# Performance work log

Measured on AMD Instinct MI355X. Metric: run time of the kernel, lower is better.

Reference implementation:

```python
import jax, jax.numpy as jnp
import numpy as np

N, E, T = 10000, 160000, 1600000
D, C, H = 256, 64, 1024  # d_model, d_message/channels, 4*d_model ffn hidden


def setup_inputs() -> dict:
    key = jax.random.key(0)
    ks = jax.random.split(key, 20)
    rn = lambda k, s, sc=1.0: jax.random.normal(k, s, dtype=jnp.float32) * sc
    return {
        "x": rn(ks[0], (N, D)),
        "y": rn(ks[1], (E, D)),
        "r": rn(ks[2], (E, 3)),
        "src": jax.random.randint(ks[3], (E,), 0, N),
        "dst": jax.random.randint(ks[4], (E,), 0, N),
        "tsrc": jax.random.randint(ks[5], (T,), 0, E),
        "tdst": jax.random.randint(ks[6], (T,), 0, E),
        "W_src": rn(ks[7], (D, C), 0.05), "b_src": rn(ks[8], (C,), 0.05),
        "W_dst": rn(ks[9], (D, C), 0.05), "b_dst": rn(ks[10], (C,), 0.05),
        "W_edge": rn(ks[11], (D, C), 0.05), "b_edge": rn(ks[12], (C,), 0.05),
        "attn": rn(ks[13], (C,), 0.05),
        "W1": rn(ks[14], (C, H), 0.05), "b1": rn(ks[15], (H,), 0.05),
        "W2": rn(ks[16], (H, D), 0.05), "b2": rn(ks[17], (D,), 0.05),
    }


def reference(x, y, r, src, dst, tsrc, tdst,
              W_src, b_src, W_dst, b_dst, W_edge, b_edge,
              attn, W1, b1, W2, b2):
    # per-bond message: xij = Lin_src(x)[src] + Lin_dst(x)[dst] + Lin_edge(y)  -> (E, C)
    xij = (x @ W_src + b_src)[src] + (x @ W_dst + b_dst)[dst] + (y @ W_edge + b_edge)

    # triplet angle cosine via normalized (negated) bond vectors  -> (T,)
    rnorm = -r / jnp.linalg.norm(r, axis=1, keepdims=True)
    cos_jik = jnp.clip(jnp.sum(rnorm[tsrc] * rnorm[tdst], axis=-1), -1.0 + 1e-6, 1.0 - 1e-6)

    # Chebyshev expansion: T_n(cos) = cos(n * arccos(cos))  -> (T, C)
    n = jnp.arange(C, dtype=jnp.float32)
    z_jik = jnp.cos(n[None, :] * jnp.arccos(cos_jik)[:, None])

    # triplet feature and attention logit
    e_jik = jax.nn.silu(z_jik + xij[tsrc] + xij[tdst])          # (T, C)
    logits = e_jik @ attn                                        # (T,)

    # segment softmax over triplets grouped by destination bond (edge_softmax)
    mx = jax.ops.segment_max(logits, tdst, num_segments=E)
    ex = jnp.exp(logits - mx[tdst])
    den = jax.ops.segment_sum(ex, tdst, num_segments=E)
    a = ex / den[tdst]                                           # (T,)

    # attention-weighted scatter-sum of neighbor bond features  -> (E, C)
    ft = jax.ops.segment_sum(xij[tsrc] * a[:, None], tdst, num_segments=E)

    # feedforward: Linear -> SiLU -> Linear  -> (E, D)
    return jax.nn.silu(ft @ W1 + b1) @ W2 + b2
```

## Files before the change

### kernel.cpp

```cpp
#include <hip/hip_runtime.h>

#define N_NODES 10000
#define N_EDGES 160000
#define N_TRI   1600000
#define DM      256
#define CH      64
#define HH      1024

typedef short bf16x8 __attribute__((ext_vector_type(8)));
typedef float f32x4  __attribute__((ext_vector_type(4)));

__device__ __forceinline__ unsigned short f2bf(float f) {
  unsigned int u = __float_as_uint(f);
  u += 0x7fff + ((u >> 16) & 1);
  return (unsigned short)(u >> 16);
}

__global__ __launch_bounds__(256) void k_node_proj(
    const float* __restrict__ x, const float* __restrict__ Ws, const float* __restrict__ bs,
    const float* __restrict__ Wd, const float* __restrict__ bd,
    float* __restrict__ xs, float* __restrict__ xd) {
  __shared__ float xl[4][DM];
  int tid = threadIdx.x;
  int n0 = blockIdx.x * 4;
  for (int i = tid; i < 4 * DM; i += 256) xl[i >> 8][i & 255] = x[n0 * DM + i];
  __syncthreads();
  int c = tid & 63, g = tid >> 6;
  float as = bs[c], ad = bd[c];
  for (int d = 0; d < DM; d++) {
    float xv = xl[g][d];
    as += xv * Ws[d * CH + c];
    ad += xv * Wd[d * CH + c];
  }
  int n = n0 + g;
  xs[n * CH + c] = as;
  xd[n * CH + c] = ad;
}

__global__ __launch_bounds__(256) void k_edge_proj(
    const float* __restrict__ y, const float* __restrict__ We, const float* __restrict__ be,
    const float* __restrict__ xs, const float* __restrict__ xd,
    const int* __restrict__ src, const int* __restrict__ dst,
    float* __restrict__ xij) {
  __shared__ float yl[16][DM];
  int tid = threadIdx.x;
  int e0 = blockIdx.x * 16;
  for (int i = tid; i < 16 * DM; i += 256) yl[i >> 8][i & 255] = y[e0 * DM + i];
  __syncthreads();
  int c = tid & 63, g = tid >> 6;
  float acc[4];
#pragma unroll
  for (int s = 0; s < 4; s++) acc[s] = be[c];
  for (int d = 0; d < DM; d += 4) {
    float w0 = We[(d + 0) * CH + c];
    float w1 = We[(d + 1) * CH + c];
    float w2 = We[(d + 2) * CH + c];
    float w3 = We[(d + 3) * CH + c];
#pragma unroll
    for (int s = 0; s < 4; s++) {
      const float4 yv = *(const float4*)&yl[g * 4 + s][d];
      acc[s] += yv.x * w0 + yv.y * w1 + yv.z * w2 + yv.w * w3;
    }
  }
#pragma unroll
  for (int s = 0; s < 4; s++) {
    int e = e0 + g * 4 + s;
    xij[e * CH + c] = acc[s] + xs[src[e] * CH + c] + xd[dst[e] * CH + c];
  }
}

__global__ void k_rnorm(const float* __restrict__ r, float4* __restrict__ rn4) {
  int e = blockIdx.x * 256 + threadIdx.x;
  if (e >= N_EDGES) return;
  float a = r[e * 3 + 0], b = r[e * 3 + 1], c = r[e * 3 + 2];
  float inv = rsqrtf(a * a + b * b + c * c);
  rn4[e] = (float4){-a * inv, -b * inv, -c * inv, 0.f};
}

__global__ __launch_bounds__(256) void k_theta(
    const float4* __restrict__ rn4, const int* __restrict__ tsrc, const int* __restrict__ tdst,
    float* __restrict__ theta) {
  int t = blockIdx.x * 256 + threadIdx.x;
  if (t >= N_TRI) return;
  float4 a = rn4[tsrc[t]];
  float4 b = rn4[tdst[t]];
  float c = a.x * b.x + a.y * b.y + a.z * b.z;
  c = fminf(fmaxf(c, -1.0f + 1e-6f), 1.0f - 1e-6f);
  theta[t] = acosf(c);
}

__global__ void k_hist(const int* __restrict__ tdst, int* __restrict__ cnt) {
  int t = blockIdx.x * 256 + threadIdx.x;
  if (t < N_TRI) atomicAdd(&cnt[tdst[t]], 1);
}

__global__ __launch_bounds__(256) void k_scan_sum(const int* __restrict__ cnt,
                                                  int* __restrict__ bsum, int n) {
  __shared__ int s[256];
  int b = blockIdx.x, tid = threadIdx.x;
  int tot = 0;
#pragma unroll
  for (int i = 0; i < 8; i++) {
    int idx = b * 2048 + i * 256 + tid;
    if (idx < n) tot += cnt[idx];
  }
  s[tid] = tot;
  __syncthreads();
  for (int off = 128; off > 0; off >>= 1) {
    if (tid < off) s[tid] += s[tid + off];
    __syncthreads();
  }
  if (tid == 0) bsum[b] = s[0];
}

__global__ void k_scan_top(int* __restrict__ bsum, int nb, int* __restrict__ start_last) {
  if (threadIdx.x == 0) {
    int run = 0;
    for (int i = 0; i < nb; i++) {
      int v = bsum[i];
      bsum[i] = run;
      run += v;
    }
    *start_last = run;
  }
}

__global__ __launch_bounds__(256) void k_scan_apply(const int* __restrict__ cnt,
                                                    const int* __restrict__ bsum,
                                                    int* __restrict__ start,
                                                    int* __restrict__ cur, int n) {
  __shared__ int s[256];
  int b = blockIdx.x, tid = threadIdx.x;
  int base = b * 2048 + tid * 8;
  int loc[8];
  int tot = 0;
#pragma unroll
  for (int i = 0; i < 8; i++) {
    int idx = base + i;
    int v = (idx < n) ? cnt[idx] : 0;
    loc[i] = tot;
    tot += v;
  }
  s[tid] = tot;
  __syncthreads();
  for (int off = 1; off < 256; off <<= 1) {
    int t2 = 0;
    if (tid >= off) t2 = s[tid - off];
    __syncthreads();
    if (tid >= off) s[tid] += t2;
    __syncthreads();
  }
  int excl = s[tid] - tot + bsum[b];
#pragma unroll
  for (int i = 0; i < 8; i++) {
    int idx = base + i;
    if (idx < n) {
      int v = excl + loc[i];
      start[idx] = v;
      cur[idx] = v;
    }
  }
}

__global__ void k_scatter(const int* __restrict__ tdst, int* __restrict__ cur,
                          int* __restrict__ sorted) {
  int t = blockIdx.x * 256 + threadIdx.x;
  if (t < N_TRI) {
    int p = atomicAdd(&cur[tdst[t]], 1);
    sorted[p] = t;
  }
}

__global__ __launch_bounds__(256) void k_attn_ft(
    const int* __restrict__ start, const int* __restrict__ sorted,
    const float* __restrict__ theta, const int* __restrict__ tsrc,
    const float* __restrict__ xij, const float* __restrict__ attn,
    unsigned short* __restrict__ ft) {
  int tid = threadIdx.x;
  int e = blockIdx.x * 4 + (tid >> 6);
  int lane = tid & 63;
  float lanef = (float)lane;
  int beg = start[e], end = start[e + 1];
  int deg = end - beg;
  float xd = xij[e * CH + lane];
  float av = attn[lane];
  float m = -1e30f, den = 0.f, acc = 0.f;
  if (deg > 0 && deg <= 64) {
    int ts_ = 0;
    float th_ = 0.f;
    if (lane < deg) {
      int t = sorted[beg + lane];
      ts_ = tsrc[t];
      th_ = theta[t];
    }
    int ts_cur = __shfl(ts_, 0);
    float th_cur = __shfl(th_, 0);
    float xs_cur = xij[ts_cur * CH + lane];
    for (int i = 0; i < deg; i++) {
      float th_nxt = 0.f, xs_nxt = 0.f;
      if (i + 1 < deg) {
        int ts_nxt = __shfl(ts_, i + 1);
        th_nxt = __shfl(th_, i + 1);
        xs_nxt = xij[ts_nxt * CH + lane];
      }
      float v = __cosf(th_cur * lanef) + xs_cur + xd;
      float sv = v / (1.0f + __expf(-v));
      float contrib = sv * av;
#pragma unroll
      for (int off = 32; off; off >>= 1) contrib += __shfl_xor(contrib, off);
      float mn = fmaxf(m, contrib);
      float scale = __expf(m - mn);
      float p = __expf(contrib - mn);
      den = den * scale + p;
      acc = acc * scale + p * xs_cur;
      m = mn;
      th_cur = th_nxt;
      xs_cur = xs_nxt;
    }
  } else if (deg > 64) {
    for (int i = 0; i < deg; i++) {
      int t = sorted[beg + i];
      int ts = tsrc[t];
      float th = theta[t];
      float xs = xij[ts * CH + lane];
      float v = __cosf(th * lanef) + xs + xd;
      float sv = v / (1.0f + __expf(-v));
      float contrib = sv * av;
#pragma unroll
      for (int off = 32; off; off >>= 1) contrib += __shfl_xor(contrib, off);
      float mn = fmaxf(m, contrib);
      float scale = __expf(m - mn);
      float p = __expf(contrib - mn);
      den = den * scale + p;
      acc = acc * scale + p * xs;
      m = mn;
    }
  }
  ft[e * CH + lane] = f2bf(deg > 0 ? acc / den : 0.f);
}

__global__ __launch_bounds__(256) void k_prep_w1p(const float* __restrict__ W1,
                                                  unsigned short* __restrict__ W1P) {
  int idx = blockIdx.x * 256 + threadIdx.x;
  int k = idx & 63, row = idx >> 6;
  int i = row & 15, t = (row >> 4) & 1, hb = row >> 5;
  int hidden = hb * 32 + ((i >> 2) << 3) + (t << 2) + (i & 3);
  W1P[idx] = f2bf(W1[k * HH + hidden]);
}

__global__ __launch_bounds__(256) void k_prep_w2t(const float* __restrict__ W2,
                                                  unsigned short* __restrict__ W2T) {
  int idx = blockIdx.x * 256 + threadIdx.x;
  int n = idx >> 10, k = idx & 1023;
  W2T[idx] = f2bf(W2[k * DM + n]);
}

__global__ __launch_bounds__(256, 3) void k_ffn_mfma5(
    const unsigned short* __restrict__ ft, const unsigned short* __restrict__ W1P,
    const float* __restrict__ b1, const unsigned short* __restrict__ W2T,
    const float* __restrict__ b2, float* __restrict__ out) {
  __shared__ __align__(16) unsigned short hbuf[2][4 * 64 * 8];
  int tid = threadIdx.x;
  int w = tid >> 6, lane = tid & 63;
  int l16 = lane & 15, q = lane >> 4;
  int e0 = blockIdx.x * 64;

  bf16x8 ftf[2];
#pragma unroll
  for (int s = 0; s < 2; s++)
    ftf[s] = *(const bf16x8*)&ft[(size_t)(e0 + w * 16 + l16) * CH + s * 32 + q * 8];

  f32x4 acc[4][4];
#pragma unroll
  for (int mt = 0; mt < 4; mt++)
#pragma unroll
    for (int nt = 0; nt < 4; nt++) acc[mt][nt] = (f32x4){0.f, 0.f, 0.f, 0.f};

  bf16x8 w1f[2][2];
#pragma unroll
  for (int t = 0; t < 2; t++)
#pragma unroll
    for (int s = 0; s < 2; s++)
      w1f[t][s] = *(const bf16x8*)&W1P[(size_t)(t * 16 + l16) * 64 + s * 32 + q * 8];

  bf16x8 bwc[4];
#pragma unroll
  for (int nt = 0; nt < 4; nt++)
    bwc[nt] = *(const bf16x8*)&W2T[(size_t)(w * 64 + nt * 16 + l16) * HH + q * 8];

  int p = 0;
  for (int hb = 0; hb < 32; hb++) {
    int hbn = (hb < 31) ? hb + 1 : 31;
    bf16x8 bwn[4];
#pragma unroll
    for (int nt = 0; nt < 4; nt++)
      bwn[nt] = *(const bf16x8*)&W2T[(size_t)(w * 64 + nt * 16 + l16) * HH + hbn * 32 + q * 8];
    bf16x8 w1n[2][2];
#pragma unroll
    for (int t = 0; t < 2; t++)
#pragma unroll
      for (int s = 0; s < 2; s++)
        w1n[t][s] = *(const bf16x8*)&W1P[(size_t)((hbn * 2 + t) * 16 + l16) * 64 + s * 32 + q * 8];

    f32x4 h0 = (f32x4){0.f, 0.f, 0.f, 0.f};
    f32x4 h1 = (f32x4){0.f, 0.f, 0.f, 0.f};
    h0 = __builtin_amdgcn_mfma_f32_16x16x32_bf16(w1f[0][0], ftf[0], h0, 0, 0, 0);
    h0 = __builtin_amdgcn_mfma_f32_16x16x32_bf16(w1f[0][1], ftf[1], h0, 0, 0, 0);
    h1 = __builtin_amdgcn_mfma_f32_16x16x32_bf16(w1f[1][0], ftf[0], h1, 0, 0, 0);
    h1 = __builtin_amdgcn_mfma_f32_16x16x32_bf16(w1f[1][1], ftf[1], h1, 0, 0, 0);

    const float4 bv0 = *(const float4*)&b1[hb * 32 + q * 8];
    const float4 bv1 = *(const float4*)&b1[hb * 32 + q * 8 + 4];
    float v0 = h0[0] + bv0.x, v1 = h0[1] + bv0.y, v2 = h0[2] + bv0.z, v3 = h0[3] + bv0.w;
    float u0 = h1[0] + bv1.x, u1 = h1[1] + bv1.y, u2 = h1[2] + bv1.z, u3 = h1[3] + bv1.w;
    float s0 = v0 / (1.f + __expf(-v0)), s1 = v1 / (1.f + __expf(-v1));
    float s2 = v2 / (1.f + __expf(-v2)), s3 = v3 / (1.f + __expf(-v3));
    float t0 = u0 / (1.f + __expf(-u0)), t1 = u1 / (1.f + __expf(-u1));
    float t2 = u2 / (1.f + __expf(-u2)), t3 = u3 / (1.f + __expf(-u3));
    union { bf16x8 v; unsigned int u[4]; } pa;
    pa.u[0] = ((unsigned int)f2bf(s1) << 16) | f2bf(s0);
    pa.u[1] = ((unsigned int)f2bf(s3) << 16) | f2bf(s2);
    pa.u[2] = ((unsigned int)f2bf(t1) << 16) | f2bf(t0);
    pa.u[3] = ((unsigned int)f2bf(t3) << 16) | f2bf(t2);
    *(bf16x8*)&hbuf[p][(w * 64 + lane) * 8] = pa.v;

    __syncthreads();

    bf16x8 pam[4];
#pragma unroll
    for (int mt = 0; mt < 4; mt++)
      pam[mt] = *(const bf16x8*)&hbuf[p][(mt * 64 + lane) * 8];
#pragma unroll
    for (int nt = 0; nt < 4; nt++)
#pragma unroll
      for (int mt = 0; mt < 4; mt++)
        acc[mt][nt] = __builtin_amdgcn_mfma_f32_16x16x32_bf16(pam[mt], bwc[nt], acc[mt][nt], 0, 0, 0);

#pragma unroll
    for (int nt = 0; nt < 4; nt++) bwc[nt] = bwn[nt];
#pragma unroll
    for (int t = 0; t < 2; t++)
#pragma unroll
      for (int s = 0; s < 2; s++) w1f[t][s] = w1n[t][s];
    p ^= 1;
  }

#pragma unroll
  for (int nt = 0; nt < 4; nt++) {
    int col = w * 64 + nt * 16 + l16;
    float b2v = b2[col];
#pragma unroll
    for (int mt = 0; mt < 4; mt++) {
      int erow = e0 + mt * 16 + q * 4;
#pragma unroll
      for (int r = 0; r < 4; r++)
        out[(size_t)(erow + r) * DM + col] = acc[mt][nt][r] + b2v;
    }
  }
}

extern "C" void kernel_launch(void* const* d_in, const int* in_sizes, int n_in,
                              void* d_out, int out_size, void* d_ws, size_t ws_size,
                              hipStream_t stream) {
  (void)in_sizes; (void)n_in; (void)out_size; (void)ws_size;
  const float* x      = (const float*)d_in[0];
  const float* y      = (const float*)d_in[1];
  const float* r      = (const float*)d_in[2];
  const int*   src    = (const int*)d_in[3];
  const int*   dst    = (const int*)d_in[4];
  const int*   tsrc   = (const int*)d_in[5];
  const int*   tdst   = (const int*)d_in[6];
  const float* W_src  = (const float*)d_in[7];
  const float* b_src  = (const float*)d_in[8];
  const float* W_dst  = (const float*)d_in[9];
  const float* b_dst  = (const float*)d_in[10];
  const float* W_edge = (const float*)d_in[11];
  const float* b_edge = (const float*)d_in[12];
  const float* attn   = (const float*)d_in[13];
  const float* W1     = (const float*)d_in[14];
  const float* b1     = (const float*)d_in[15];
  const float* W2     = (const float*)d_in[16];
  const float* b2     = (const float*)d_in[17];
  float* out = (float*)d_out;

  char* wsp = (char*)d_ws;
  auto alloc = [&](size_t bytes) -> char* {
    char* p = wsp;
    wsp += (bytes + 255) & ~(size_t)255;
    return p;
  };
  float* xs     = (float*)alloc((size_t)N_NODES * CH * 4);
  float* xd     = (float*)alloc((size_t)N_NODES * CH * 4);
  float* xij    = (float*)alloc((size_t)N_EDGES * CH * 4);
  float4* rn4   = (float4*)alloc((size_t)N_EDGES * 16);
  float* theta  = (float*)alloc((size_t)N_TRI * 4);
  int*   cnt    = (int*)alloc((size_t)N_EDGES * 4);
  int*   start  = (int*)alloc((size_t)(N_EDGES + 1) * 4);
  int*   cur    = (int*)alloc((size_t)N_EDGES * 4);
  int*   bsum   = (int*)alloc(1024 * 4);
  int*   sorted = (int*)alloc((size_t)N_TRI * 4);
  unsigned short* ftb = (unsigned short*)alloc((size_t)N_EDGES * CH * 2);
  unsigned short* W1P = (unsigned short*)alloc((size_t)CH * HH * 2);
  unsigned short* W2T = (unsigned short*)alloc((size_t)HH * DM * 2);

  const int NB = (N_EDGES + 2047) / 2048;

  k_prep_w1p<<<(CH * HH) / 256, 256, 0, stream>>>(W1, W1P);
  k_prep_w2t<<<(HH * DM) / 256, 256, 0, stream>>>(W2, W2T);

  k_node_proj<<<N_NODES / 4, 256, 0, stream>>>(x, W_src, b_src, W_dst, b_dst, xs, xd);
  k_rnorm<<<N_EDGES / 256, 256, 0, stream>>>(r, rn4);
  k_edge_proj<<<N_EDGES / 16, 256, 0, stream>>>(y, W_edge, b_edge, xs, xd, src, dst, xij);
  k_theta<<<N_TRI / 256, 256, 0, stream>>>(rn4, tsrc, tdst, theta);

  hipMemsetAsync(cnt, 0, (size_t)N_EDGES * 4, stream);
  k_hist<<<N_TRI / 256, 256, 0, stream>>>(tdst, cnt);
  k_scan_sum<<<NB, 256, 0, stream>>>(cnt, bsum, N_EDGES);
  k_scan_top<<<1, 64, 0, stream>>>(bsum, NB, &start[N_EDGES]);
  k_scan_apply<<<NB, 256, 0, stream>>>(cnt, bsum, start, cur, N_EDGES);
  k_scatter<<<N_TRI / 256, 256, 0, stream>>>(tdst, cur, sorted);

  k_attn_ft<<<N_EDGES / 4, 256, 0, stream>>>(start, sorted, theta, tsrc, xij, attn, ftb);
  k_ffn_mfma5<<<N_EDGES / 64, 256, 0, stream>>>(ftb, W1P, b1, W2T, b2, out);
}
```

Measured before the change: 1.244 ms.

## Split fused FFN into two GEMM kernels with chunked hidden buffer

The fused FFN kernel, which computed the hidden activation per 64-edge tile and immediately consumed it through shared memory with a barrier each step, is replaced by two kernels per 40000-edge chunk. The first writes the bf16 SiLU hidden activations to a global workspace in MFMA fragment layout. The second reads them back and does the W2 GEMM, with the output columns split across two blocks. This removes the per-step __syncthreads and exposes more parallelism, but adds a global round trip of the hidden tensor (about 80 MB per chunk) and extra kernel launches.

```diff
diff --git a/kernel.cpp b/kernel.cpp
--- a/kernel.cpp
+++ b/kernel.cpp
@@ -6,6 +6,7 @@
 #define DM      256
 #define CH      64
 #define HH      1024
+#define ECHUNK  40000
 
 typedef short bf16x8 __attribute__((ext_vector_type(8)));
 typedef float f32x4  __attribute__((ext_vector_type(4)));
@@ -255,99 +256,92 @@
   W2T[idx] = f2bf(W2[k * DM + n]);
 }
 
-__global__ __launch_bounds__(256, 3) void k_ffn_mfma5(
+__global__ __launch_bounds__(256) void k_ffn_g1(
     const unsigned short* __restrict__ ft, const unsigned short* __restrict__ W1P,
-    const float* __restrict__ b1, const unsigned short* __restrict__ W2T,
-    const float* __restrict__ b2, float* __restrict__ out) {
-  __shared__ __align__(16) unsigned short hbuf[2][4 * 64 * 8];
+    const float* __restrict__ b1, unsigned short* __restrict__ hpk) {
   int tid = threadIdx.x;
   int w = tid >> 6, lane = tid & 63;
   int l16 = lane & 15, q = lane >> 4;
-  int e0 = blockIdx.x * 64;
-
-  bf16x8 ftf[2];
-#pragma unroll
-  for (int s = 0; s < 2; s++)
-    ftf[s] = *(const bf16x8*)&ft[(size_t)(e0 + w * 16 + l16) * CH + s * 32 + q * 8];
-
-  f32x4 acc[4][4];
+  int tile = blockIdx.x;
+  int e0 = tile * 64;
+
+  bf16x8 ftf[4][2];
 #pragma unroll
   for (int mt = 0; mt < 4; mt++)
 #pragma unroll
-    for (int nt = 0; nt < 4; nt++) acc[mt][nt] = (f32x4){0.f, 0.f, 0.f, 0.f};
-
-  bf16x8 w1f[2][2];
-#pragma unroll
-  for (int t = 0; t < 2; t++)
-#pragma unroll
     for (int s = 0; s < 2; s++)
-      w1f[t][s] = *(const bf16x8*)&W1P[(size_t)(t * 16 + l16) * 64 + s * 32 + q * 8];
-
-  bf16x8 bwc[4];
-#pragma unroll
-  for (int nt = 0; nt < 4; nt++)
-    bwc[nt] = *(const bf16x8*)&W2T[(size_t)(w * 64 + nt * 16 + l16) * HH + q * 8];
-
-  int p = 0;
-  for (int hb = 0; hb < 32; hb++) {
-    int hbn = (hb < 31) ? hb + 1 : 31;
-    bf16x8 bwn[4];
-#pragma unroll
-    for (int nt = 0; nt < 4; nt++)
-      bwn[nt] = *(const bf16x8*)&W2T[(size_t)(w * 64 + nt * 16 + l16) * HH + hbn * 32 + q * 8];
-    bf16x8 w1n[2][2];
+      ftf[mt][s] = *(const bf16x8*)&ft[(size_t)(e0 + mt * 16 + l16) * CH + s * 32 + q * 8];
+
+#pragma unroll
+  for (int hbl = 0; hbl < 2; hbl++) {
+    int hb = blockIdx.y * 8 + w * 2 + hbl;
+    bf16x8 w1f[2][2];
 #pragma unroll
     for (int t = 0; t < 2; t++)
 #pragma unroll
       for (int s = 0; s < 2; s++)
-        w1n[t][s] = *(const bf16x8*)&W1P[(size_t)((hbn * 2 + t) * 16 + l16) * 64 + s * 32 + q * 8];
-
-    f32x4 h0 = (f32x4){0.f, 0.f, 0.f, 0.f};
-    f32x4 h1 = (f32x4){0.f, 0.f, 0.f, 0.f};
-    h0 = __builtin_amdgcn_mfma_f32_16x16x32_bf16(w1f[0][0], ftf[0], h0, 0, 0, 0);
-    h0 = __builtin_amdgcn_mfma_f32_16x16x32_bf16(w1f[0][1], ftf[1], h0, 0, 0, 0);
-    h1 = __builtin_amdgcn_mfma_f32_16x16x32_bf16(w1f[1][0], ftf[0], h1, 0, 0, 0);
-    h1 = __builtin_amdgcn_mfma_f32_16x16x32_bf16(w1f[1][1], ftf[1], h1, 0, 0, 0);
-
+        w1f[t][s] = *(const bf16x8*)&W1P[(size_t)((hb * 2 + t) * 16 + l16) * 64 + s * 32 + q * 8];
     const float4 bv0 = *(const float4*)&b1[hb * 32 + q * 8];
     const float4 bv1 = *(const float4*)&b1[hb * 32 + q * 8 + 4];
-    float v0 = h0[0] + bv0.x, v1 = h0[1] + bv0.y, v2 = h0[2] + bv0.z, v3 = h0[3] + bv0.w;
-    float u0 = h1[0] + bv1.x, u1 = h1[1] + bv1.y, u2 = h1[2] + bv1.z, u3 = h1[3] + bv1.w;
-    float s0 = v0 / (1.f + __expf(-v0)), s1 = v1 / (1.f + __expf(-v1));
-    float s2 = v2 / (1.f + __expf(-v2)), s3 = v3 / (1.f + __expf(-v3));
-    float t0 = u0 / (1.f + __expf(-u0)), t1 = u1 / (1.f + __expf(-u1));
-    float t2 = u2 / (1.f + __expf(-u2)), t3 = u3 / (1.f + __expf(-u3));
-    union { bf16x8 v; unsigned int u[4]; } pa;
-    pa.u[0] = ((unsigned int)f2bf(s1) << 16) | f2bf(s0);
-    pa.u[1] = ((unsigned int)f2bf(s3) << 16) | f2bf(s2);
-    pa.u[2] = ((unsigned int)f2bf(t1) << 16) | f2bf(t0);
-    pa.u[3] = ((unsigned int)f2bf(t3) << 16) | f2bf(t2);
-    *(bf16x8*)&hbuf[p][(w * 64 + lane) * 8] = pa.v;
-
-    __syncthreads();
-
-    bf16x8 pam[4];
+#pragma unroll
+    for (int mt = 0; mt < 4; mt++) {
+      f32x4 h0 = (f32x4){0.f, 0.f, 0.f, 0.f};
+      f32x4 h1 = (f32x4){0.f, 0.f, 0.f, 0.f};
+      h0 = __builtin_amdgcn_mfma_f32_16x16x32_bf16(w1f[0][0], ftf[mt][0], h0, 0, 0, 0);
+      h0 = __builtin_amdgcn_mfma_f32_16x16x32_bf16(w1f[0][1], ftf[mt][1], h0, 0, 0, 0);
+      h1 = __builtin_amdgcn_mfma_f32_16x16x32_bf16(w1f[1][0], ftf[mt][0], h1, 0, 0, 0);
+      h1 = __builtin_amdgcn_mfma_f32_16x16x32_bf16(w1f[1][1], ftf[mt][1], h1, 0, 0, 0);
+      float v0 = h0[0] + bv0.x, v1 = h0[1] + bv0.y, v2 = h0[2] + bv0.z, v3 = h0[3] + bv0.w;
+      float u0 = h1[0] + bv1.x, u1 = h1[1] + bv1.y, u2 = h1[2] + bv1.z, u3 = h1[3] + bv1.w;
+      float s0 = v0 / (1.f + __expf(-v0)), s1 = v1 / (1.f + __expf(-v1));
+      float s2 = v2 / (1.f + __expf(-v2)), s3 = v3 / (1.f + __expf(-v3));
+      float t0 = u0 / (1.f + __expf(-u0)), t1 = u1 / (1.f + __expf(-u1));
+      float t2 = u2 / (1.f + __expf(-u2)), t3 = u3 / (1.f + __expf(-u3));
+      union { bf16x8 v; unsigned int u[4]; } pa;
+      pa.u[0] = ((unsigned int)f2bf(s1) << 16) | f2bf(s0);
+      pa.u[1] = ((unsigned int)f2bf(s3) << 16) | f2bf(s2);
+      pa.u[2] = ((unsigned int)f2bf(t1) << 16) | f2bf(t0);
+      pa.u[3] = ((unsigned int)f2bf(t3) << 16) | f2bf(t2);
+      *(bf16x8*)&hpk[((((size_t)tile * 32 + hb) * 4 + mt) * 64 + lane) * 8] = pa.v;
+    }
+  }
+}
+
+__global__ __launch_bounds__(128) void k_ffn_g2(
+    const unsigned short* __restrict__ hpk, const unsigned short* __restrict__ W2T,
+    const float* __restrict__ b2, float* __restrict__ out) {
+  int tid = threadIdx.x;
+  int w = tid >> 6, lane = tid & 63;
+  int l16 = lane & 15, q = lane >> 4;
+  int tile = blockIdx.x >> 1;
+  int ch = blockIdx.x & 1;
+  int colBase = ch * 128 + w * 64;
+  int e0 = tile * 64;
+
+  f32x4 acc[4][4];
+#pragma unroll
+  for (int mt = 0; mt < 4; mt++)
+#pragma unroll
+    for (int nt = 0; nt < 4; nt++) acc[mt][nt] = (f32x4){0.f, 0.f, 0.f, 0.f};
+
+  for (int hb = 0; hb < 32; hb++) {
+    bf16x8 pam[4], bw[4];
 #pragma unroll
     for (int mt = 0; mt < 4; mt++)
-      pam[mt] = *(const bf16x8*)&hbuf[p][(mt * 64 + lane) * 8];
+      pam[mt] = *(const bf16x8*)&hpk[((((size_t)tile * 32 + hb) * 4 + mt) * 64 + lane) * 8];
 #pragma unroll
     for (int nt = 0; nt < 4; nt++)
+      bw[nt] = *(const bf16x8*)&W2T[(size_t)(colBase + nt * 16 + l16) * HH + hb * 32 + q * 8];
+#pragma unroll
+    for (int nt = 0; nt < 4; nt++)
 #pragma unroll
       for (int mt = 0; mt < 4; mt++)
-        acc[mt][nt] = __builtin_amdgcn_mfma_f32_16x16x32_bf16(pam[mt], bwc[nt], acc[mt][nt], 0, 0, 0);
-
-#pragma unroll
-    for (int nt = 0; nt < 4; nt++) bwc[nt] = bwn[nt];
-#pragma unroll
-    for (int t = 0; t < 2; t++)
-#pragma unroll
-      for (int s = 0; s < 2; s++) w1f[t][s] = w1n[t][s];
-    p ^= 1;
+        acc[mt][nt] = __builtin_amdgcn_mfma_f32_16x16x32_bf16(pam[mt], bw[nt], acc[mt][nt], 0, 0, 0);
   }
 
 #pragma unroll
   for (int nt = 0; nt < 4; nt++) {
-    int col = w * 64 + nt * 16 + l16;
+    int col = colBase + nt * 16 + l16;
     float b2v = b2[col];
 #pragma unroll
     for (int mt = 0; mt < 4; mt++) {
@@ -402,6 +396,7 @@
   unsigned short* ftb = (unsigned short*)alloc((size_t)N_EDGES * CH * 2);
   unsigned short* W1P = (unsigned short*)alloc((size_t)CH * HH * 2);
   unsigned short* W2T = (unsigned short*)alloc((size_t)HH * DM * 2);
+  unsigned short* hpk = (unsigned short*)alloc((size_t)ECHUNK * HH * 2);
 
   const int NB = (N_EDGES + 2047) / 2048;
 
@@ -421,5 +416,11 @@
   k_scatter<<<N_TRI / 256, 256, 0, stream>>>(tdst, cur, sorted);
 
   k_attn_ft<<<N_EDGES / 4, 256, 0, stream>>>(start, sorted, theta, tsrc, xij, attn, ftb);
-  k_ffn_mfma5<<<N_EDGES / 64, 256, 0, stream>>>(ftb, W1P, b1, W2T, b2, out);
-}
+
+  const int TILES = ECHUNK / 64;
+  for (int c = 0; c < N_EDGES / ECHUNK; c++) {
+    const size_t E0 = (size_t)c * ECHUNK;
+    k_ffn_g1<<<dim3(TILES, 4), 256, 0, stream>>>(ftb + E0 * CH, W1P, b1, hpk);
+    k_ffn_g2<<<TILES * 2, 128, 0, stream>>>(hpk, W2T, b2, out + E0 * DM);
+  }
+}
```

Result: no change. 1.260 ms (+1.2%).
